# Performance work log

Hardware: AMD Instinct MI355X
Metric: run time of the kernel (lower is better)

## Reference

```python
import jax, jax.numpy as jnp
import numpy as np
import math

B, S, E = 2, 2048, 2048
H, NOPE, ROPE, V, KVR, DOWN = 16, 64, 32, 64, 256, 2
QKD = NOPE + ROPE
SCALE = QKD ** -0.5
LOW = 4


def setup_inputs() -> dict:
    key = jax.random.key(0)
    ks = jax.random.split(key, 8)
    def w(k, shape):
        return jax.random.normal(k, shape, jnp.float32) * 0.02
    return {
        "hidden_states": jax.random.normal(ks[0], (B, S, E), jnp.float32),
        "wq": w(ks[1], (H * QKD, E)),
        "wkv_a": w(ks[2], (KVR + ROPE, E)),
        "kv_ln_g": jnp.ones((KVR,), jnp.float32),
        "kv_ln_b": jnp.zeros((KVR,), jnp.float32),
        "wkv_b": w(ks[3], (H * (NOPE + V), KVR)),
        "wo": w(ks[4], (E, H * V)),
        "fc_c_w": w(ks[5], (KVR // LOW, KVR)),
        "fc_c_b": jnp.zeros((KVR // LOW,), jnp.float32),
        "fc_p_w": w(ks[6], (KVR // LOW, KVR)),
        "fc_p_b": jnp.zeros((KVR // LOW,), jnp.float32),
    }


def _layernorm(x, g, b, eps=1e-5):
    m = jnp.mean(x, -1, keepdims=True)
    v = jnp.var(x, -1, keepdims=True)
    return (x - m) * jax.lax.rsqrt(v + eps) * g + b


def _pos_enc(T, d):
    # sinusoidal PE: even dims sin, odd dims cos (interleaved)
    pos = jnp.arange(T, dtype=jnp.float32)[:, None]
    div = jnp.exp(jnp.arange(0, d, 2, dtype=jnp.float32) * (-math.log(10000.0) / d))
    ang = pos * div[None, :]
    return jnp.stack([jnp.sin(ang), jnp.cos(ang)], -1).reshape(T, d)


def _rope(x, cos, sin):
    # complex multiply on adjacent pairs, matching torch.view_as_complex path
    xr = x.reshape(x.shape[:-1] + (-1, 2))
    x0, x1 = xr[..., 0], xr[..., 1]
    return jnp.stack([x0 * cos - x1 * sin, x0 * sin + x1 * cos], -1).reshape(x.shape)


def reference(hidden_states, wq, wkv_a, kv_ln_g, kv_ln_b, wkv_b, wo,
              fc_c_w, fc_c_b, fc_p_w, fc_p_b):
    # q projection -> split nope / rope parts
    q = (hidden_states @ wq.T).reshape(B, S, H, QKD)
    q_nope, q_pe = q[..., :NOPE], q[..., NOPE:]
    # low-rank kv projection -> latent + shared rope key
    kv = hidden_states @ wkv_a.T
    kv_c, k_pe = kv[..., :KVR], kv[..., KVR:]
    kv_c = _layernorm(kv_c, kv_ln_g, kv_ln_b)
    # inline partial RoPE (position_ids = arange)
    pos = jnp.arange(S, dtype=jnp.float32)
    freqs = 1.0 / (10000.0 ** (jnp.arange(0, ROPE, 2, dtype=jnp.float32) / ROPE))
    ang = pos[:, None] * freqs[None, :]  # (S, ROPE//2)
    cos, sin = jnp.cos(ang), jnp.sin(ang)
    q_pe = _rope(q_pe, cos[None, :, None, :], sin[None, :, None, :])
    k_pe = _rope(k_pe, cos[None, :, :], sin[None, :, :])
    # hypernetwork gate (train path): C from downsampled PE, repeat_interleave
    t = -(-S // DOWN)
    P = _pos_enc(S, KVR)
    C = jnp.repeat(_pos_enc(t, KVR), DOWN, axis=0)[:S]
    C2 = C @ fc_c_w.T + fc_c_b
    P2 = P @ fc_p_w.T + fc_p_b
    Wg = jax.nn.sigmoid(C2 @ P2.T)  # (S, S)
    r = jnp.arange(S)
    chunk = ((r[:, None] // DOWN) == (r[None, :] // DOWN)) & \
            ((r[:, None] % DOWN) >= (r[None, :] % DOWN))
    Wg = Wg * chunk.astype(Wg.dtype)
    # temporally merged latent KV (simulated compressed cache)
    kv_t = jnp.einsum('ts,bsc->btc', Wg, kv_c)
    k_pe_t = jnp.einsum('ts,bsr->btr', Wg, k_pe)
    # absorbed wkv_b: q_nope into latent space
    wkv_b3 = wkv_b.reshape(H, NOPE + V, KVR)
    q_abs = jnp.einsum('bshd,hdc->bshc', q_nope, wkv_b3[:, :NOPE])
    scores = (jnp.einsum('bshc,btc->bsht', q_abs, kv_t)
              + jnp.einsum('bshr,btr->bsht', q_pe, k_pe_t)) * SCALE
    # stride-aware causal mask: chunk-boundary keys + diagonal
    visible = ((r[None, :] <= r[:, None]) & (((r[None, :] + 1) % DOWN) == 0)) | \
              (r[None, :] == r[:, None])
    mask = jnp.where(visible, 0.0, -1e9).astype(scores.dtype)
    attn = jax.nn.softmax(scores + mask[:, None, :], axis=-1)
    x = jnp.einsum('bsht,btc->bshc', attn, kv_t)
    out = jnp.einsum('bshc,hdc->bshd', x, wkv_b3[:, NOPE:]).reshape(B, S, H * V)
    return out @ wo.T
```

## Files before the change

kernel.cpp:

```cpp
#include <hip/hip_runtime.h>
#include <hip/hip_bf16.h>
#include <math.h>
#include <stdint.h>

#define B_ 2
#define S_ 2048
#define E_ 2048
#define H_ 16
#define NOPE_ 64
#define ROPE_ 32
#define V_ 64
#define KVR_ 256
#define QKD_ 96
#define SCALE_ 0.10206207261596577f

typedef __hip_bfloat16 bf16;
typedef __attribute__((ext_vector_type(8))) short short8;
typedef __attribute__((ext_vector_type(4))) short short4v;
typedef __attribute__((ext_vector_type(4))) float floatx4;

__device__ __forceinline__ float bf2f(bf16 v) { return __bfloat162float(v); }
__device__ __forceinline__ float s2f(short v) {
    bf16 h = *reinterpret_cast<bf16*>(&v);
    return __bfloat162float(h);
}
__device__ __forceinline__ short f2bf_s(float f) {
    bf16 h = __float2bfloat16(f);
    return *reinterpret_cast<short*>(&h);
}
__device__ __forceinline__ void store_c(float* C, size_t i, float v) { C[i] = v; }
__device__ __forceinline__ void store_c(bf16* C, size_t i, float v) { C[i] = __float2bfloat16(v); }

__device__ __forceinline__ void g2l16(const bf16* g, bf16* l) {
    __builtin_amdgcn_global_load_lds(
        (const __attribute__((address_space(1))) void*)g,
        (__attribute__((address_space(3))) void*)l,
        16, 0, 0);
}

#define CV_N0 1048576
#define CV_N1 (CV_N0 + 393216)
#define CV_N2 (CV_N1 + 262144)
#define CV_N3 (CV_N2 + 65536)
#define CV_N4 (CV_N3 + 98304)
#define CV_N5 (CV_N4 + 32768)
__global__ __launch_bounds__(256) void conv_fused_kernel(const float* __restrict__ hs,
                                                         const float* __restrict__ wq,
                                                         const float* __restrict__ wo,
                                                         const float* __restrict__ wkv_b,
                                                         const float* __restrict__ wkv_a,
                                                         bf16* __restrict__ hs_bf,
                                                         bf16* __restrict__ wq_bf,
                                                         bf16* __restrict__ wo_bf,
                                                         bf16* __restrict__ wkvb_bf,
                                                         bf16* __restrict__ wkva_pad,
                                                         bf16* __restrict__ wkvbT) {
    int i = blockIdx.x * 256 + threadIdx.x;
    const float* src;
    bf16* dst;
    int j;
    if (i < CV_N0)      { src = hs;    dst = hs_bf;   j = i; }
    else if (i < CV_N1) { src = wq;    dst = wq_bf;   j = i - CV_N0; }
    else if (i < CV_N2) { src = wo;    dst = wo_bf;   j = i - CV_N1; }
    else if (i < CV_N3) { src = wkv_b; dst = wkvb_bf; j = i - CV_N2; }
    else if (i < CV_N4) {
        j = i - CV_N3;
        int row = j >> 8;
        short8 r;
        if (row < 288) {
            float4 a = ((const float4*)wkv_a)[2 * j];
            float4 b = ((const float4*)wkv_a)[2 * j + 1];
            r[0] = f2bf_s(a.x); r[1] = f2bf_s(a.y); r[2] = f2bf_s(a.z); r[3] = f2bf_s(a.w);
            r[4] = f2bf_s(b.x); r[5] = f2bf_s(b.y); r[6] = f2bf_s(b.z); r[7] = f2bf_s(b.w);
        } else {
            for (int k = 0; k < 8; ++k) r[k] = 0;
        }
        ((short8*)wkva_pad)[j] = r;
        return;
    } else if (i < CV_N5) {
        j = i - CV_N4;
        int h = j >> 11;
        int rem = j & 2047;
        int d0 = (rem >> 8) * 8;
        int c = rem & 255;
        short8 v;
#pragma unroll
        for (int jj = 0; jj < 8; ++jj)
            v[jj] = f2bf_s(wkv_b[(size_t)(h * 128 + d0 + jj) * 256 + c]);
        *(short8*)(void*)&wkvbT[((size_t)h * 256 + c) * 64 + d0] = v;
        return;
    } else return;
    float4 a = ((const float4*)src)[2 * j];
    float4 b = ((const float4*)src)[2 * j + 1];
    short8 r;
    r[0] = f2bf_s(a.x); r[1] = f2bf_s(a.y); r[2] = f2bf_s(a.z); r[3] = f2bf_s(a.w);
    r[4] = f2bf_s(b.x); r[5] = f2bf_s(b.y); r[6] = f2bf_s(b.z); r[7] = f2bf_s(b.w);
    ((short8*)dst)[j] = r;
}

template <typename TC>
__global__ __launch_bounds__(256, 2) void gemm_bt_lds(const bf16* __restrict__ A,
                                                      const bf16* __restrict__ Bm,
                                                      TC* __restrict__ C,
                                                      int M, int N, int K) {
    __shared__ bf16 Asf[128 * 32];
    __shared__ bf16 Bsf[128 * 32];
    int tid = threadIdx.x;
    int lane = tid & 63, w = tid >> 6;
    int q4 = lane >> 4, c16 = lane & 15;
    int wr = w >> 1, wc = w & 1;
    int m0 = blockIdx.y * 128, n0 = blockIdx.x * 128;
    floatx4 acc[4][4];
#pragma unroll
    for (int mi = 0; mi < 4; ++mi)
#pragma unroll
        for (int ni = 0; ni < 4; ++ni) acc[mi][ni] = (floatx4){0.f, 0.f, 0.f, 0.f};

    for (int k0 = 0; k0 < K; k0 += 32) {
        __syncthreads();
#pragma unroll
        for (int i = 0; i < 2; ++i) {
            int c = (w << 6) + lane + i * 256;
            int row = c >> 2, kc = c & 3;
            g2l16(&A[(size_t)(m0 + row) * K + k0 + kc * 8], &Asf[c * 8]);
            g2l16(&Bm[(size_t)(n0 + row) * K + k0 + kc * 8], &Bsf[c * 8]);
        }
        __syncthreads();
        short8 af[4], bfr[4];
#pragma unroll
        for (int mi = 0; mi < 4; ++mi)
            af[mi] = *(const short8*)(const void*)&Asf[(wr * 64 + mi * 16 + c16) * 32 + q4 * 8];
#pragma unroll
        for (int ni = 0; ni < 4; ++ni)
            bfr[ni] = *(const short8*)(const void*)&Bsf[(wc * 64 + ni * 16 + c16) * 32 + q4 * 8];
#pragma unroll
        for (int mi = 0; mi < 4; ++mi)
#pragma unroll
            for (int ni = 0; ni < 4; ++ni)
                acc[mi][ni] = __builtin_amdgcn_mfma_f32_16x16x32_bf16(af[mi], bfr[ni], acc[mi][ni], 0, 0, 0);
    }
#pragma unroll
    for (int mi = 0; mi < 4; ++mi)
#pragma unroll
        for (int ni = 0; ni < 4; ++ni)
#pragma unroll
            for (int r = 0; r < 4; ++r) {
                int row = m0 + wr * 64 + mi * 16 + q4 * 4 + r;
                int col = n0 + wc * 64 + ni * 16 + c16;
                store_c(C, (size_t)row * N + col, acc[mi][ni][r]);
            }
}

__global__ __launch_bounds__(256) void gemm_qkv_fused64(const bf16* __restrict__ A,
                                                        const bf16* __restrict__ Bq,
                                                        const bf16* __restrict__ Bkv,
                                                        bf16* __restrict__ Cq,
                                                        float* __restrict__ Ckv,
                                                        int K) {
    int bid = blockIdx.x;
    int orig = (bid & 7) * 120 + (bid >> 3);
    int by = orig / 15, bx = orig % 15;
    bool isq = bx < 12;
    const bf16* Bm = isq ? Bq : Bkv;
    int n0 = isq ? bx * 128 : (bx - 12) * 128;
    int m0 = by * 64;
    __shared__ bf16 Asf[64 * 32];
    __shared__ bf16 Bsf[128 * 32];
    int tid = threadIdx.x;
    int lane = tid & 63, w = tid >> 6;
    int q4 = lane >> 4, c16 = lane & 15;
    int wr = w >> 1, wc = w & 1;
    floatx4 acc[2][4];
#pragma unroll
    for (int mi = 0; mi < 2; ++mi)
#pragma unroll
        for (int ni = 0; ni < 4; ++ni) acc[mi][ni] = (floatx4){0.f, 0.f, 0.f, 0.f};

    for (int k0 = 0; k0 < K; k0 += 32) {
        __syncthreads();
        {
            int c = tid;
            int row = c >> 2, kc = c & 3;
            g2l16(&A[(size_t)(m0 + row) * K + k0 + kc * 8], &Asf[c * 8]);
        }
#pragma unroll
        for (int i = 0; i < 2; ++i) {
            int c = tid + i * 256;
            int row = c >> 2, kc = c & 3;
            g2l16(&Bm[(size_t)(n0 + row) * K + k0 + kc * 8], &Bsf[c * 8]);
        }
        __syncthreads();
        short8 af[2], bfr[4];
#pragma unroll
        for (int mi = 0; mi < 2; ++mi)
            af[mi] = *(const short8*)(const void*)&Asf[(wr * 32 + mi * 16 + c16) * 32 + q4 * 8];
#pragma unroll
        for (int ni = 0; ni < 4; ++ni)
            bfr[ni] = *(const short8*)(const void*)&Bsf[(wc * 64 + ni * 16 + c16) * 32 + q4 * 8];
#pragma unroll
        for (int mi = 0; mi < 2; ++mi)
#pragma unroll
            for (int ni = 0; ni < 4; ++ni)
                acc[mi][ni] = __builtin_amdgcn_mfma_f32_16x16x32_bf16(af[mi], bfr[ni], acc[mi][ni], 0, 0, 0);
    }
#pragma unroll
    for (int mi = 0; mi < 2; ++mi)
#pragma unroll
        for (int ni = 0; ni < 4; ++ni)
#pragma unroll
            for (int r = 0; r < 4; ++r) {
                int row = m0 + wr * 32 + mi * 16 + q4 * 4 + r;
                int col = n0 + wc * 64 + ni * 16 + c16;
                if (isq)
                    Cq[(size_t)row * 1536 + col] = __float2bfloat16(acc[mi][ni][r]);
                else
                    Ckv[(size_t)row * 384 + col] = acc[mi][ni][r];
            }
}

template <typename TC>
__global__ __launch_bounds__(256, 4) void gemm64_lds(const bf16* __restrict__ A, int lda, int aoffz,
                                                     const bf16* __restrict__ Bm, int ldb, int boffz,
                                                     TC* __restrict__ C, int ldc, int coffz,
                                                     int K, float scale) {
    int z = blockIdx.z;
    A += (size_t)z * aoffz;
    Bm += (size_t)z * boffz;
    C += (size_t)z * coffz;
    __shared__ bf16 Asf[64 * 32];
    __shared__ bf16 Bsf[64 * 32];
    int tid = threadIdx.x;
    int lane = tid & 63, w = tid >> 6;
    int q4 = lane >> 4, c16 = lane & 15;
    int m0 = blockIdx.y * 64, n0 = blockIdx.x * 64;
    floatx4 acc[4];
#pragma unroll
    for (int ni = 0; ni < 4; ++ni) acc[ni] = (floatx4){0.f, 0.f, 0.f, 0.f};
    int row = tid >> 2, kc = tid & 3;
    for (int k0 = 0; k0 < K; k0 += 32) {
        __syncthreads();
        g2l16(&A[(size_t)(m0 + row) * lda + k0 + kc * 8], &Asf[tid * 8]);
        g2l16(&Bm[(size_t)(n0 + row) * ldb + k0 + kc * 8], &Bsf[tid * 8]);
        __syncthreads();
        short8 af = *(const short8*)(const void*)&Asf[(w * 16 + c16) * 32 + q4 * 8];
#pragma unroll
        for (int ni = 0; ni < 4; ++ni) {
            short8 bfr = *(const short8*)(const void*)&Bsf[(ni * 16 + c16) * 32 + q4 * 8];
            acc[ni] = __builtin_amdgcn_mfma_f32_16x16x32_bf16(af, bfr, acc[ni], 0, 0, 0);
        }
    }
#pragma unroll
    for (int ni = 0; ni < 4; ++ni)
#pragma unroll
        for (int rr = 0; rr < 4; ++rr)
            store_c(C, (size_t)(m0 + w * 16 + q4 * 4 + rr) * ldc + n0 + ni * 16 + c16,
                    acc[ni][rr] * scale);
}

__global__ __launch_bounds__(64) void c2p2g_kernel(const float* __restrict__ fcw_c,
                                                   const float* __restrict__ fcb_c,
                                                   const float* __restrict__ fcw_p,
                                                   const float* __restrict__ fcb_p,
                                                   float* __restrict__ g0,
                                                   float* __restrict__ g1) {
    int t = blockIdx.x;
    int k = threadIdx.x;
    __shared__ float Crow[256], Prow[256], Pprev[256];
    for (int i = k; i < 128; i += 64) {
        float div = expf(-(float)i * 0.07195578415606393f);
        float ap = (float)t * div;
        Prow[2 * i]     = sinf(ap);
        Prow[2 * i + 1] = cosf(ap);
        float ac = (float)(t >> 1) * div;
        Crow[2 * i]     = sinf(ac);
        Crow[2 * i + 1] = cosf(ac);
        float app = (float)(t - 1) * div;
        Pprev[2 * i]     = sinf(app);
        Pprev[2 * i + 1] = cosf(app);
    }
    __syncthreads();
    float sc = fcb_c[k], sp = fcb_p[k], spp = fcb_p[k];
    for (int c = 0; c < 256; ++c) {
        float wc_ = fcw_c[(size_t)k * 256 + c];
        float wp_ = fcw_p[(size_t)k * 256 + c];
        sc += Crow[c] * wc_;
        sp += Prow[c] * wp_;
        spp += Pprev[c] * wp_;
    }
    float d0 = sc * sp, d1 = sc * spp;
#pragma unroll
    for (int o = 32; o; o >>= 1) {
        d0 += __shfl_down(d0, o);
        d1 += __shfl_down(d1, o);
    }
    if (k == 0) {
        g0[t] = 1.0f / (1.0f + expf(-d0));
        g1[t] = (t & 1) ? 1.0f / (1.0f + expf(-d1)) : 0.f;
    }
}

__global__ __launch_bounds__(256) void lnkve_kernel(const float* __restrict__ kvraw,
                                                    const float* __restrict__ g,
                                                    const float* __restrict__ bta,
                                                    const float* __restrict__ g0,
                                                    const float* __restrict__ g1,
                                                    bf16* __restrict__ kve_full,
                                                    bf16* __restrict__ kvo) {
    int pb = blockIdx.x;
    int b = pb >> 10, u = pb & 1023;
    int t0 = 2 * u, t1 = 2 * u + 1;
    size_t r0 = (size_t)b * S_ + t0, r1 = r0 + 1;
    int tid = threadIdx.x;
    int lane = tid & 63, w = tid >> 6;
    float x0 = kvraw[r0 * 384 + tid];
    float x1 = kvraw[r1 * 384 + tid];
    float s0 = x0, q0 = x0 * x0, s1 = x1, q1 = x1 * x1;
#pragma unroll
    for (int o = 32; o; o >>= 1) {
        s0 += __shfl_down(s0, o); q0 += __shfl_down(q0, o);
        s1 += __shfl_down(s1, o); q1 += __shfl_down(q1, o);
    }
    __shared__ float red[4][4];
    __shared__ float st[4];
    if (lane == 0) { red[w][0] = s0; red[w][1] = q0; red[w][2] = s1; red[w][3] = q1; }
    __syncthreads();
    if (tid == 0) {
        float S0 = red[0][0] + red[1][0] + red[2][0] + red[3][0];
        float Q0 = red[0][1] + red[1][1] + red[2][1] + red[3][1];
        float S1 = red[0][2] + red[1][2] + red[2][2] + red[3][2];
        float Q1 = red[0][3] + red[1][3] + red[2][3] + red[3][3];
        float m0 = S0 / 256.0f, m1 = S1 / 256.0f;
        st[0] = m0; st[1] = rsqrtf(Q0 / 256.0f - m0 * m0 + 1e-5f);
        st[2] = m1; st[3] = rsqrtf(Q1 / 256.0f - m1 * m1 + 1e-5f);
    }
    __syncthreads();
    float gg = g[tid], bb_ = bta[tid];
    float y0 = (x0 - st[0]) * st[1] * gg + bb_;
    float y1 = (x1 - st[2]) * st[3] * gg + bb_;
    float a0 = g0[t0], a1 = g0[t1], b1 = g1[t1];
    kve_full[r0 * 288 + tid] = __float2bfloat16(a0 * y0);
    float vo = a1 * y1 + b1 * y0;
    bf16 vob = __float2bfloat16(vo);
    kve_full[r1 * 288 + tid] = vob;
    kvo[((size_t)b * 1024 + u) * 296 + tid] = vob;
    if (tid < 16) {
        int j = tid;
        float freq = expf(-(float)(2 * j) * 0.28782313662425572f);
        float a00 = (float)t0 * freq, a01 = (float)t1 * freq;
        float c0 = cosf(a00), sn0 = sinf(a00);
        float c1 = cosf(a01), sn1 = sinf(a01);
        float e00 = kvraw[r0 * 384 + 256 + 2 * j], e01 = kvraw[r0 * 384 + 256 + 2 * j + 1];
        float e10 = kvraw[r1 * 384 + 256 + 2 * j], e11 = kvraw[r1 * 384 + 256 + 2 * j + 1];
        float k00 = e00 * c0 - e01 * sn0, k01 = e00 * sn0 + e01 * c0;
        float k10 = e10 * c1 - e11 * sn1, k11 = e10 * sn1 + e11 * c1;
        kve_full[r0 * 288 + 256 + 2 * j]     = __float2bfloat16(a0 * k00);
        kve_full[r0 * 288 + 256 + 2 * j + 1] = __float2bfloat16(a0 * k01);
        float u0 = a1 * k10 + b1 * k00, u1 = a1 * k11 + b1 * k01;
        bf16 u0b = __float2bfloat16(u0), u1b = __float2bfloat16(u1);
        kve_full[r1 * 288 + 256 + 2 * j]     = u0b;
        kve_full[r1 * 288 + 256 + 2 * j + 1] = u1b;
        kvo[((size_t)b * 1024 + u) * 296 + 256 + 2 * j]     = u0b;
        kvo[((size_t)b * 1024 + u) * 296 + 256 + 2 * j + 1] = u1b;
    }
}

__global__ __launch_bounds__(256) void kvoT32_kernel(const bf16* __restrict__ kvo,
                                                     bf16* __restrict__ kvoT) {
    int uch = blockIdx.x, b = blockIdx.y;
    int c = threadIdx.x;
    const bf16* src = kvo + ((size_t)b * 1024 + uch * 32) * 296 + c;
    short v[32];
#pragma unroll
    for (int j = 0; j < 32; ++j) v[j] = *(const short*)&src[(size_t)j * 296];
    bf16* dst = kvoT + (((size_t)b * 32 + uch) * 256 + c) * 32;
    int swz = (c >> 1) & 3;
#pragma unroll
    for (int q = 0; q < 4; ++q) {
        short8 o;
#pragma unroll
        for (int jj = 0; jj < 8; ++jj)
            o[jj] = (jj < 4) ? v[4 * q + jj] : v[16 + 4 * q + (jj - 4)];
        *(short8*)(void*)&dst[(q ^ swz) * 8] = o;
    }
}

__global__ __launch_bounds__(256) void rope_qe_kernel(const bf16* __restrict__ q,
                                                      bf16* __restrict__ qe) {
    int idx = blockIdx.x * 256 + threadIdx.x;
    if (idx >= B_ * S_ * H_ * 16) return;
    int j = idx & 15;
    int s = (idx >> 8) & (S_ - 1);
    float freq = expf(-(float)(2 * j) * 0.28782313662425572f);
    float ang = (float)s * freq;
    float c = cosf(ang), sn = sinf(ang);
    size_t row = idx >> 4;
    float a0 = bf2f(q[row * QKD_ + NOPE_ + 2 * j]);
    float a1 = bf2f(q[row * QKD_ + NOPE_ + 2 * j + 1]);
    qe[row * 288 + 256 + 2 * j]     = __float2bfloat16((a0 * c - a1 * sn) * SCALE_);
    qe[row * 288 + 256 + 2 * j + 1] = __float2bfloat16((a0 * sn + a1 * c) * SCALE_);
}

__global__ __launch_bounds__(256, 2) void attn8_kernel(const bf16* __restrict__ qe,
                                                       const bf16* __restrict__ kvo,
                                                       const bf16* __restrict__ kvoT,
                                                       const bf16* __restrict__ kve_full,
                                                       bf16* __restrict__ xout) {
    int s0 = (int)(gridDim.x - 1 - blockIdx.x) * 4;
    int b = blockIdx.y;
    int tid = threadIdx.x;
    int lane = tid & 63, w = tid >> 6;
    int q4 = lane >> 4, c16 = lane & 15;
    int s = s0 + w;
    int Nodd = (s + 1) >> 1;
    int NoddMax = (s0 + 4) >> 1;
    int niter = (NoddMax + 31) >> 5;

    __shared__ bf16 kvos[2][32][296];
    __shared__ bf16 kvts[2][256][32];
    __shared__ bf16 selfr[4][288];

    const bf16* kvob = kvo + (size_t)b * 1024 * 296;
    const bf16* kvoTb = kvoT + (size_t)b * 32 * 8192;

    if (tid < 144) {
        int rr = tid / 36, ch = tid - rr * 36;
        *(short8*)(void*)&selfr[rr][ch * 8] =
            *(const short8*)(const void*)&kve_full[(size_t)(b * S_ + s0 + rr) * 288 + ch * 8];
    }

    short8 qf[9];
    const bf16* qrow = qe + ((size_t)(b * S_ + s) * H_ + c16) * 288;
#pragma unroll
    for (int kk = 0; kk < 9; ++kk) qf[kk] = *(const short8*)(const void*)&qrow[kk * 32 + q4 * 8];

    floatx4 acc[16];
#pragma unroll
    for (int n = 0; n < 16; ++n) acc[n] = (floatx4){0.f, 0.f, 0.f, 0.f};
    float m_i = -1e30f, l_i = 0.f;
    int swz = (c16 >> 1) & 3;

    auto stage = [&](int t, int p) {
        const bf16* sa = kvob + (size_t)t * 32 * 296;
        bf16* la = &kvos[p][0][0];
#pragma unroll
        for (int i = 0; i < 4; ++i)
            g2l16(&sa[(size_t)(tid + i * 256) * 8], &la[(size_t)(tid + i * 256) * 8]);
        if (tid < 160) g2l16(&sa[(size_t)(tid + 1024) * 8], &la[(size_t)(tid + 1024) * 8]);
        const bf16* sb = kvoTb + (size_t)t * 8192;
        bf16* lb = &kvts[p][0][0];
#pragma unroll
        for (int i = 0; i < 4; ++i)
            g2l16(&sb[(size_t)(tid + i * 256) * 8], &lb[(size_t)(tid + i * 256) * 8]);
    };

    stage(0, 0);
    __syncthreads();

    float sdot = 0.f;
#pragma unroll
    for (int kk = 0; kk < 9; ++kk) {
        short8 kv8 = *(const short8*)(const void*)&selfr[w][kk * 32 + q4 * 8];
#pragma unroll
        for (int j = 0; j < 8; ++j) sdot += s2f(qf[kk][j]) * s2f(kv8[j]);
    }
    sdot += __shfl_xor(sdot, 16);
    sdot += __shfl_xor(sdot, 32);

    for (int it = 0; it < niter; ++it) {
        int p = it & 1;
        if (it + 1 < niter) stage(it + 1, 1 - p);

        int u0 = it * 32;
        floatx4 ca0 = (floatx4){0.f, 0.f, 0.f, 0.f}, ca1 = (floatx4){0.f, 0.f, 0.f, 0.f};
        floatx4 cb0 = (floatx4){0.f, 0.f, 0.f, 0.f}, cb1 = (floatx4){0.f, 0.f, 0.f, 0.f};
        __builtin_amdgcn_s_setprio(1);
#pragma unroll
        for (int kk = 0; kk < 9; ++kk) {
            short8 avA = *(const short8*)(const void*)&kvos[p][c16][kk * 32 + q4 * 8];
            short8 avB = *(const short8*)(const void*)&kvos[p][16 + c16][kk * 32 + q4 * 8];
            if (kk & 1) {
                ca1 = __builtin_amdgcn_mfma_f32_16x16x32_bf16(avA, qf[kk], ca1, 0, 0, 0);
                cb1 = __builtin_amdgcn_mfma_f32_16x16x32_bf16(avB, qf[kk], cb1, 0, 0, 0);
            } else {
                ca0 = __builtin_amdgcn_mfma_f32_16x16x32_bf16(avA, qf[kk], ca0, 0, 0, 0);
                cb0 = __builtin_amdgcn_mfma_f32_16x16x32_bf16(avB, qf[kk], cb0, 0, 0, 0);
            }
        }
        __builtin_amdgcn_s_setprio(0);
        floatx4 cA = ca0 + ca1;
        floatx4 cB = cb0 + cb1;
        int kA = u0 + q4 * 4;
        int kB = u0 + 16 + q4 * 4;
#pragma unroll
        for (int r = 0; r < 4; ++r) {
            if (kA + r >= Nodd) cA[r] = -1e30f;
            if (kB + r >= Nodd) cB[r] = -1e30f;
        }
        float tmax = fmaxf(fmaxf(fmaxf(cA[0], cA[1]), fmaxf(cA[2], cA[3])),
                           fmaxf(fmaxf(cB[0], cB[1]), fmaxf(cB[2], cB[3])));
        tmax = fmaxf(tmax, __shfl_xor(tmax, 16));
        tmax = fmaxf(tmax, __shfl_xor(tmax, 32));
        float mn = fmaxf(m_i, tmax);
        bool chg = mn > m_i;
        float al = __expf(m_i - mn);
        float pA0 = __expf(cA[0] - mn), pA1 = __expf(cA[1] - mn);
        float pA2 = __expf(cA[2] - mn), pA3 = __expf(cA[3] - mn);
        float pB0 = __expf(cB[0] - mn), pB1 = __expf(cB[1] - mn);
        float pB2 = __expf(cB[2] - mn), pB3 = __expf(cB[3] - mn);
        float rs = (pA0 + pA1 + pA2 + pA3) + (pB0 + pB1 + pB2 + pB3);
        rs += __shfl_xor(rs, 16);
        rs += __shfl_xor(rs, 32);
        l_i = l_i * al + rs;
        m_i = mn;
        if (__any(chg)) {
#pragma unroll
            for (int n = 0; n < 16; ++n) {
                acc[n][0] *= al; acc[n][1] *= al; acc[n][2] *= al; acc[n][3] *= al;
            }
        }
        short8 pf;
        pf[0] = f2bf_s(pA0); pf[1] = f2bf_s(pA1); pf[2] = f2bf_s(pA2); pf[3] = f2bf_s(pA3);
        pf[4] = f2bf_s(pB0); pf[5] = f2bf_s(pB1); pf[6] = f2bf_s(pB2); pf[7] = f2bf_s(pB3);
        __builtin_amdgcn_s_setprio(1);
#pragma unroll
        for (int n = 0; n < 16; ++n) {
            short8 a8 = *(const short8*)(const void*)&kvts[p][n * 16 + c16][(q4 ^ swz) * 8];
            acc[n] = __builtin_amdgcn_mfma_f32_16x16x32_bf16(a8, pf, acc[n], 0, 0, 0);
        }
        __builtin_amdgcn_s_setprio(0);
        __syncthreads();
    }

    if ((s & 1) == 0) {
        float mn = fmaxf(m_i, sdot);
        float al = __expf(m_i - mn);
        float pp = __expf(sdot - mn);
        l_i = l_i * al + pp;
        m_i = mn;
#pragma unroll
        for (int n = 0; n < 16; ++n) {
            short4v kv4 = *(const short4v*)(const void*)&selfr[w][n * 16 + q4 * 4];
#pragma unroll
            for (int r = 0; r < 4; ++r)
                acc[n][r] = acc[n][r] * al + pp * s2f(kv4[r]);
        }
    }

    float invl = 1.0f / l_i;
    bf16* orow = xout + ((size_t)(b * S_ + s) * H_ + c16) * 256;
#pragma unroll
    for (int n = 0; n < 16; ++n) {
        short4v o;
        o[0] = f2bf_s(acc[n][0] * invl);
        o[1] = f2bf_s(acc[n][1] * invl);
        o[2] = f2bf_s(acc[n][2] * invl);
        o[3] = f2bf_s(acc[n][3] * invl);
        *(short4v*)(void*)&orow[n * 16 + q4 * 4] = o;
    }
}

extern "C" void kernel_launch(void* const* d_in, const int* in_sizes, int n_in,
                              void* d_out, int out_size, void* d_ws, size_t ws_size,
                              hipStream_t stream) {
    const float* hs     = (const float*)d_in[0];
    const float* wq     = (const float*)d_in[1];
    const float* wkv_a  = (const float*)d_in[2];
    const float* ln_g   = (const float*)d_in[3];
    const float* ln_b   = (const float*)d_in[4];
    const float* wkv_b  = (const float*)d_in[5];
    const float* wo     = (const float*)d_in[6];
    const float* fc_c_w = (const float*)d_in[7];
    const float* fc_c_b = (const float*)d_in[8];
    const float* fc_p_w = (const float*)d_in[9];
    const float* fc_p_b = (const float*)d_in[10];
    float* out = (float*)d_out;
    (void)in_sizes; (void)n_in; (void)out_size; (void)ws_size;

    const int M = B_ * S_;
    char* wsb = (char*)d_ws;
    size_t o = 0;
    auto alloc = [&](size_t bytes) { char* p = wsb + o; o += (bytes + 255) & ~(size_t)255; return p; };

    bf16* qe = (bf16*)alloc((size_t)M * H_ * 288 * 2);
    char* region2 = alloc((size_t)M * H_ * 256 * 2);
    bf16* hs_bf    = (bf16*)region2;
    bf16* wq_bf    = (bf16*)(region2 + (size_t)M * E_ * 2);
    bf16* wkva_pad = (bf16*)(region2 + (size_t)M * E_ * 2 + (size_t)1536 * E_ * 2);
    bf16* x_bf     = (bf16*)region2;
    char* region3 = alloc((size_t)M * 1536 * 2);
    bf16* q_bf    = (bf16*)region3;
    bf16* outp_bf = (bf16*)region3;
    float* kvraw = (float*)alloc((size_t)M * 384 * 4);
    bf16* wo_bf   = (bf16*)alloc((size_t)E_ * 1024 * 2);
    bf16* wkvb_bf = (bf16*)alloc((size_t)2048 * 256 * 2);
    bf16* wkvbT   = (bf16*)alloc((size_t)H_ * 256 * 64 * 2);
    bf16* kve_full = (bf16*)alloc((size_t)M * 288 * 2);
    bf16* kvo      = (bf16*)alloc((size_t)B_ * 1024 * 296 * 2);
    bf16* kvoT     = (bf16*)alloc((size_t)B_ * 32 * 8192 * 2);
    float* g0 = (float*)alloc(S_ * 4);
    float* g1 = (float*)alloc(S_ * 4);

    conv_fused_kernel<<<(CV_N5 + 255) / 256, 256, 0, stream>>>(
        hs, wq, wo, wkv_b, wkv_a, hs_bf, wq_bf, wo_bf, wkvb_bf, wkva_pad, wkvbT);
    gemm_qkv_fused64<<<960, 256, 0, stream>>>(hs_bf, wq_bf, wkva_pad, q_bf, kvraw, E_);
    c2p2g_kernel<<<S_, 64, 0, stream>>>(fc_c_w, fc_c_b, fc_p_w, fc_p_b, g0, g1);
    lnkve_kernel<<<B_ * 1024, 256, 0, stream>>>(kvraw, ln_g, ln_b, g0, g1, kve_full, kvo);
    kvoT32_kernel<<<dim3(32, B_), 256, 0, stream>>>(kvo, kvoT);
    gemm64_lds<bf16><<<dim3(256 / 64, M / 64, H_), 256, 0, stream>>>(
        q_bf, H_ * QKD_, QKD_, wkvbT, 64, 256 * 64, qe, H_ * 288, 288, 64, SCALE_);
    rope_qe_kernel<<<(M * H_ * 16 + 255) / 256, 256, 0, stream>>>(q_bf, qe);
    attn8_kernel<<<dim3(S_ / 4, B_), 256, 0, stream>>>(qe, kvo, kvoT, kve_full, x_bf);
    gemm64_lds<bf16><<<dim3(1, M / 64, H_), 256, 0, stream>>>(
        x_bf, H_ * 256, 256, wkvb_bf + (size_t)64 * 256, 256, 128 * 256, outp_bf, 1024, 64, 256, 1.0f);
    gemm_bt_lds<float><<<dim3(E_ / 128, M / 128), 256, 0, stream>>>(outp_bf, wo_bf, out, M, E_, 1024);
}
```

Measured before the change: 338.5 us.

## Replace LDS-staged 4-query attention blocks with single-wave blocks reading KV from global

```diff
diff --git a/kernel.cpp b/kernel.cpp
--- a/kernel.cpp
+++ b/kernel.cpp
@@ -373,14 +373,13 @@
 #pragma unroll
     for (int j = 0; j < 32; ++j) v[j] = *(const short*)&src[(size_t)j * 296];
     bf16* dst = kvoT + (((size_t)b * 32 + uch) * 256 + c) * 32;
-    int swz = (c >> 1) & 3;
 #pragma unroll
     for (int q = 0; q < 4; ++q) {
         short8 o;
 #pragma unroll
         for (int jj = 0; jj < 8; ++jj)
             o[jj] = (jj < 4) ? v[4 * q + jj] : v[16 + 4 * q + (jj - 4)];
-        *(short8*)(void*)&dst[(q ^ swz) * 8] = o;
+        *(short8*)(void*)&dst[q * 8] = o;
     }
 }
 
@@ -400,84 +399,53 @@
     qe[row * 288 + 256 + 2 * j + 1] = __float2bfloat16((a0 * sn + a1 * c) * SCALE_);
 }
 
-__global__ __launch_bounds__(256, 2) void attn8_kernel(const bf16* __restrict__ qe,
-                                                       const bf16* __restrict__ kvo,
-                                                       const bf16* __restrict__ kvoT,
-                                                       const bf16* __restrict__ kve_full,
-                                                       bf16* __restrict__ xout) {
-    int s0 = (int)(gridDim.x - 1 - blockIdx.x) * 4;
+__global__ __launch_bounds__(64) void attn9_kernel(const bf16* __restrict__ qe,
+                                                   const bf16* __restrict__ kvo,
+                                                   const bf16* __restrict__ kvoT,
+                                                   const bf16* __restrict__ kve_full,
+                                                   bf16* __restrict__ xout) {
+    int s = (int)(gridDim.x - 1 - blockIdx.x);
     int b = blockIdx.y;
-    int tid = threadIdx.x;
-    int lane = tid & 63, w = tid >> 6;
+    int lane = threadIdx.x & 63;
     int q4 = lane >> 4, c16 = lane & 15;
-    int s = s0 + w;
     int Nodd = (s + 1) >> 1;
-    int NoddMax = (s0 + 4) >> 1;
-    int niter = (NoddMax + 31) >> 5;
-
-    __shared__ bf16 kvos[2][32][296];
-    __shared__ bf16 kvts[2][256][32];
-    __shared__ bf16 selfr[4][288];
+    int niter = (Nodd + 31) >> 5;
 
     const bf16* kvob = kvo + (size_t)b * 1024 * 296;
     const bf16* kvoTb = kvoT + (size_t)b * 32 * 8192;
-
-    if (tid < 144) {
-        int rr = tid / 36, ch = tid - rr * 36;
-        *(short8*)(void*)&selfr[rr][ch * 8] =
-            *(const short8*)(const void*)&kve_full[(size_t)(b * S_ + s0 + rr) * 288 + ch * 8];
-    }
+    const bf16* kverow = kve_full + (size_t)(b * S_ + s) * 288;
 
     short8 qf[9];
     const bf16* qrow = qe + ((size_t)(b * S_ + s) * H_ + c16) * 288;
 #pragma unroll
     for (int kk = 0; kk < 9; ++kk) qf[kk] = *(const short8*)(const void*)&qrow[kk * 32 + q4 * 8];
 
+    float sdot = 0.f;
+#pragma unroll
+    for (int kk = 0; kk < 9; ++kk) {
+        short8 kv8 = *(const short8*)(const void*)&kverow[kk * 32 + q4 * 8];
+#pragma unroll
+        for (int j = 0; j < 8; ++j) sdot += s2f(qf[kk][j]) * s2f(kv8[j]);
+    }
+    sdot += __shfl_xor(sdot, 16);
+    sdot += __shfl_xor(sdot, 32);
+
     floatx4 acc[16];
 #pragma unroll
     for (int n = 0; n < 16; ++n) acc[n] = (floatx4){0.f, 0.f, 0.f, 0.f};
     float m_i = -1e30f, l_i = 0.f;
-    int swz = (c16 >> 1) & 3;
-
-    auto stage = [&](int t, int p) {
-        const bf16* sa = kvob + (size_t)t * 32 * 296;
-        bf16* la = &kvos[p][0][0];
-#pragma unroll
-        for (int i = 0; i < 4; ++i)
-            g2l16(&sa[(size_t)(tid + i * 256) * 8], &la[(size_t)(tid + i * 256) * 8]);
-        if (tid < 160) g2l16(&sa[(size_t)(tid + 1024) * 8], &la[(size_t)(tid + 1024) * 8]);
-        const bf16* sb = kvoTb + (size_t)t * 8192;
-        bf16* lb = &kvts[p][0][0];
-#pragma unroll
-        for (int i = 0; i < 4; ++i)
-            g2l16(&sb[(size_t)(tid + i * 256) * 8], &lb[(size_t)(tid + i * 256) * 8]);
-    };
-
-    stage(0, 0);
-    __syncthreads();
-
-    float sdot = 0.f;
-#pragma unroll
-    for (int kk = 0; kk < 9; ++kk) {
-        short8 kv8 = *(const short8*)(const void*)&selfr[w][kk * 32 + q4 * 8];
-#pragma unroll
-        for (int j = 0; j < 8; ++j) sdot += s2f(qf[kk][j]) * s2f(kv8[j]);
-    }
-    sdot += __shfl_xor(sdot, 16);
-    sdot += __shfl_xor(sdot, 32);
 
     for (int it = 0; it < niter; ++it) {
-        int p = it & 1;
-        if (it + 1 < niter) stage(it + 1, 1 - p);
-
         int u0 = it * 32;
+        const bf16* ka = kvob + (size_t)(u0 + c16) * 296;
+        const bf16* kb = kvob + (size_t)(u0 + 16 + c16) * 296;
         floatx4 ca0 = (floatx4){0.f, 0.f, 0.f, 0.f}, ca1 = (floatx4){0.f, 0.f, 0.f, 0.f};
         floatx4 cb0 = (floatx4){0.f, 0.f, 0.f, 0.f}, cb1 = (floatx4){0.f, 0.f, 0.f, 0.f};
         __builtin_amdgcn_s_setprio(1);
 #pragma unroll
         for (int kk = 0; kk < 9; ++kk) {
-            short8 avA = *(const short8*)(const void*)&kvos[p][c16][kk * 32 + q4 * 8];
-            short8 avB = *(const short8*)(const void*)&kvos[p][16 + c16][kk * 32 + q4 * 8];
+            short8 avA = *(const short8*)(const void*)&ka[kk * 32 + q4 * 8];
+            short8 avB = *(const short8*)(const void*)&kb[kk * 32 + q4 * 8];
             if (kk & 1) {
                 ca1 = __builtin_amdgcn_mfma_f32_16x16x32_bf16(avA, qf[kk], ca1, 0, 0, 0);
                 cb1 = __builtin_amdgcn_mfma_f32_16x16x32_bf16(avB, qf[kk], cb1, 0, 0, 0);
@@ -521,14 +489,14 @@
         short8 pf;
         pf[0] = f2bf_s(pA0); pf[1] = f2bf_s(pA1); pf[2] = f2bf_s(pA2); pf[3] = f2bf_s(pA3);
         pf[4] = f2bf_s(pB0); pf[5] = f2bf_s(pB1); pf[6] = f2bf_s(pB2); pf[7] = f2bf_s(pB3);
+        const bf16* vt = kvoTb + (size_t)it * 8192;
         __builtin_amdgcn_s_setprio(1);
 #pragma unroll
         for (int n = 0; n < 16; ++n) {
-            short8 a8 = *(const short8*)(const void*)&kvts[p][n * 16 + c16][(q4 ^ swz) * 8];
+            short8 a8 = *(const short8*)(const void*)&vt[(size_t)(n * 16 + c16) * 32 + q4 * 8];
             acc[n] = __builtin_amdgcn_mfma_f32_16x16x32_bf16(a8, pf, acc[n], 0, 0, 0);
         }
         __builtin_amdgcn_s_setprio(0);
-        __syncthreads();
     }
 
     if ((s & 1) == 0) {
@@ -539,7 +507,7 @@
         m_i = mn;
 #pragma unroll
         for (int n = 0; n < 16; ++n) {
-            short4v kv4 = *(const short4v*)(const void*)&selfr[w][n * 16 + q4 * 4];
+            short4v kv4 = *(const short4v*)(const void*)&kverow[n * 16 + q4 * 4];
 #pragma unroll
             for (int r = 0; r < 4; ++r)
                 acc[n][r] = acc[n][r] * al + pp * s2f(kv4[r]);
@@ -609,7 +577,7 @@
     gemm64_lds<bf16><<<dim3(256 / 64, M / 64, H_), 256, 0, stream>>>(
         q_bf, H_ * QKD_, QKD_, wkvbT, 64, 256 * 64, qe, H_ * 288, 288, 64, SCALE_);
     rope_qe_kernel<<<(M * H_ * 16 + 255) / 256, 256, 0, stream>>>(q_bf, qe);
-    attn8_kernel<<<dim3(S_ / 4, B_), 256, 0, stream>>>(qe, kvo, kvoT, kve_full, x_bf);
+    attn9_kernel<<<dim3(S_, B_), 64, 0, stream>>>(qe, kvo, kvoT, kve_full, x_bf);
     gemm64_lds<bf16><<<dim3(1, M / 64, H_), 256, 0, stream>>>(
         x_bf, H_ * 256, 256, wkvb_bf + (size_t)64 * 256, 256, 128 * 256, outp_bf, 1024, 64, 256, 1.0f);
     gemm_bt_lds<float><<<dim3(E_ / 128, M / 128), 256, 0, stream>>>(outp_bf, wo_bf, out, M, E_, 1024);
```

Result: slower. 420.7 us (+24.3%).
